# Optimization experiments

Hardware: AMD Instinct MI355X
Metric: run time of the kernel (lower is better)

The kernel has to match this reference:

```python
import jax, jax.numpy as jnp
import numpy as np


def _maxpool3(x):
    # 3x3 max pool, stride 1, SAME padding (NHWC), matches tf.keras MaxPooling2D
    return jax.lax.reduce_window(
        x, -jnp.inf, jax.lax.max,
        window_dimensions=(1, 3, 3, 1),
        window_strides=(1, 1, 1, 1),
        padding='SAME')


def setup_inputs() -> dict:
    key = jax.random.key(0)
    scores = jax.random.uniform(key, (16, 1024, 1024, 1), dtype=jnp.float32)
    return {"scores": scores}


def reference(scores):
    zeros = jnp.zeros_like(scores)
    max_mask = scores == _maxpool3(scores)
    for _ in range(2):
        supp_mask = _maxpool3(max_mask.astype(scores.dtype)) > 0
        supp_scores = jnp.where(supp_mask, zeros, scores)
        new_max_mask = supp_scores == _maxpool3(supp_scores)
        max_mask = max_mask | (new_max_mask & ~supp_mask)
    return jnp.where(max_mask, scores, zeros)
```

## Files before the change

### kernel.cpp

```cpp
#include <hip/hip_runtime.h>

#define IMG 1024
#define RH  16
#define NW  4
#define NEG_INF (-__builtin_inff())
#define PMASK 0x01010101u

__device__ __forceinline__ unsigned dpp_shr1_u(unsigned x) {
    return (unsigned)__builtin_amdgcn_update_dpp(0, (int)x, 0x138, 0xf, 0xf, true);
}
__device__ __forceinline__ unsigned dpp_shl1_u(unsigned x) {
    return (unsigned)__builtin_amdgcn_update_dpp(0, (int)x, 0x130, 0xf, 0xf, true);
}
__device__ __forceinline__ float dpp_shr1_f(float x) { return __uint_as_float(dpp_shr1_u(__float_as_uint(x))); }
__device__ __forceinline__ float dpp_shl1_f(float x) { return __uint_as_float(dpp_shl1_u(__float_as_uint(x))); }

__device__ __forceinline__ float max3f(float a, float b, float c) { return fmaxf(fmaxf(a, b), c); }

__device__ __forceinline__ float4 vmax3(float4 a, float4 b, float4 c) {
    return make_float4(max3f(a.x,b.x,c.x), max3f(a.y,b.y,c.y),
                       max3f(a.z,b.z,c.z), max3f(a.w,b.w,c.w));
}

__device__ __forceinline__ float4 hmax3(float4 f, float Lin, float Rin, bool l0, bool l63) {
    float sl = dpp_shr1_f(f.w);
    float sr = dpp_shl1_f(f.x);
    float L = l0 ? Lin : sl;
    float R = l63 ? Rin : sr;
    return make_float4(max3f(L,   f.x, f.y), max3f(f.x, f.y, f.z),
                       max3f(f.y, f.z, f.w), max3f(f.z, f.w, R));
}

__device__ __forceinline__ unsigned hor3(unsigned p, unsigned Lbit, unsigned Rbit, bool l0, bool l63) {
    unsigned sl = dpp_shr1_u(p);
    unsigned sr = dpp_shl1_u(p);
    unsigned L = l0 ? Lbit : ((sl >> 24) & 1u);
    unsigned R = l63 ? Rbit : (sr & 1u);
    return ((p | (p << 8) | (p >> 8)) & PMASK) | L | (R << 24);
}

__device__ __forceinline__ unsigned cmp_plane(float4 a, float4 m) {
    return (a.x == m.x ? 0x1u : 0u) | (a.y == m.y ? 0x100u : 0u) |
           (a.z == m.z ? 0x10000u : 0u) | (a.w == m.w ? 0x1000000u : 0u);
}

__device__ __forceinline__ float4 supsel(unsigned plane, float4 v) {
    return make_float4(((plane >>  0) & 1u) ? 0.f : v.x,
                       ((plane >>  8) & 1u) ? 0.f : v.y,
                       ((plane >> 16) & 1u) ? 0.f : v.z,
                       ((plane >> 24) & 1u) ? 0.f : v.w);
}

__device__ __forceinline__ float bsel(unsigned bits, int sh, float v) {
    return ((bits >> sh) & 1u) ? v : 0.f;
}

__device__ __forceinline__ unsigned vmask(int r, int lmax) {
    return ((unsigned)r < (unsigned)lmax) ? PMASK : 0u;
}

#define LDS_BARRIER() do {                                   \
    __builtin_amdgcn_sched_barrier(0);                       \
    asm volatile("s_waitcnt lgkmcnt(0)" ::: "memory");       \
    __builtin_amdgcn_s_barrier();                            \
    __builtin_amdgcn_sched_barrier(0);                       \
} while (0)

#define STEP(K, PAR) do {                                                               \
    const int s_ = sb + (K);                                                            \
    const float4 pLp = edgeR[(PAR)^1][w];                                               \
    const float4 pRp = edgeL[(PAR)^1][w + 2];                                           \
    const unsigned pLb = __float_as_uint(pLp.w);                                        \
    const unsigned pRb = __float_as_uint(pRp.w);                                        \
                                                          \
    HV[(K)+2] = hmax3(H[9+(K)], pLp.x, pRp.x, l0, l63);                                 \
                                                                    \
    float4 vm0 = vmax3(HV[(K)+2], HV[(K)+1], HV[(K)]);                                  \
    unsigned m0n = cmp_plane(H[8+(K)], vm0) & vmask(s_ - 2, lmax);                      \
    m0h = ((m0h << 1) & ~PMASK) | m0n;                                                  \
                                                                   \
    unsigned hm0n = hor3((m0h >> 1) & PMASK, pLb & 1u, pRb & 1u, l0, l63);              \
    hm0h = ((hm0h << 1) & ~PMASK) | hm0n;                                               \
                                                                 \
    unsigned s1n = (hm0h | (hm0h >> 1) | (hm0h >> 2)) & PMASK;                          \
    s1h = ((s1h << 1) & ~PMASK) | s1n;                                                  \
        \
    SS1[(K)+2] = supsel(s1n & vmask(s_ - 4, lmax), H[6+(K)]);                           \
                                                             \
    H1[(K)+2] = hmax3(SS1[(K)+1], pLp.y, pRp.y, l0, l63);                               \
                                                                 \
    float4 vm1 = vmax3(H1[(K)+2], H1[(K)+1], H1[(K)]);                                  \
    unsigned s1l2 = (s1h >> 2) & PMASK;                                                 \
    unsigned rvm6 = vmask(s_ - 6, lmax);                                                \
    unsigned nm1 = cmp_plane(SS1[(K)], vm1) & rvm6;                                     \
    unsigned mk1n = ((m0h >> 4) & PMASK) | (nm1 & ~s1l2);                               \
    mk1h = ((mk1h << 1) & ~PMASK) | mk1n;                                               \
                                                                  \
    unsigned hm1n = hor3((mk1h >> 1) & PMASK, (pLb >> 1) & 1u, (pRb >> 1) & 1u, l0, l63);\
    hm1h = ((hm1h << 1) & ~PMASK) | hm1n;                                               \
                                                                \
    unsigned s2n = (hm1h | (hm1h >> 1) | (hm1h >> 2)) & PMASK;                          \
    s2h = ((s2h << 1) & ~PMASK) | s2n;                                                  \
                           \
    SS2[(K)+2] = supsel(s2n & vmask(s_ - 8, lmax), H[2+(K)]);                           \
                                                            \
    H2[(K)+2] = hmax3(SS2[(K)+1], pLp.z, pRp.z, l0, l63);                               \
                                                      \
    float4 vm2 = vmax3(H2[(K)+2], H2[(K)+1], H2[(K)]);                                  \
    unsigned s2l2 = (s2h >> 2) & PMASK;                                                 \
    unsigned rvm10 = vmask(s_ - 10, lmax);                                              \
    unsigned nm2 = cmp_plane(SS2[(K)], vm2) & rvm10;                                    \
    unsigned mk2 = ((mk1h >> 4) & PMASK) | (nm2 & ~s2l2);                               \
    const int srow = s_ - 10;                                                           \
    if (srow >= y0 && srow < yend) {                                                    \
        float4 vv = H[(K)];                                                             \
        outp4[(size_t)srow * (IMG/4) + tid] = make_float4(                              \
            bsel(mk2, 0, vv.x), bsel(mk2, 8, vv.y),                                     \
            bsel(mk2, 16, vv.z), bsel(mk2, 24, vv.w));                                  \
    }                                                                                   \
    unsigned bitsR = ((m0n >> 24) & 1u) | (((mk1n >> 24) & 1u) << 1);                   \
    unsigned bitsL = (m0n & 1u) | ((mk1n & 1u) << 1);                                   \
    if (l63) edgeR[(PAR)][w + 1] = make_float4(H[10+(K)].w, SS1[(K)+2].w, SS2[(K)+2].w, __uint_as_float(bitsR)); \
    if (l0)  edgeL[(PAR)][w + 1] = make_float4(H[10+(K)].x, SS1[(K)+2].x, SS2[(K)+2].x, __uint_as_float(bitsL)); \
    LDS_BARRIER();                                                                      \
} while (0)

__global__ __launch_bounds__(256, 4)
void nms_sweep(const float* __restrict__ in, float* __restrict__ out)
{
    __shared__ float4 edgeR[2][NW + 2];
    __shared__ float4 edgeL[2][NW + 2];

    const int tid  = threadIdx.x;
    const int lane = tid & 63;
    const int w    = tid >> 6;
    const bool l0  = (lane == 0);
    const bool l63 = (lane == 63);
    const int y0   = (int)blockIdx.x * RH;
    const int yend = y0 + RH;
    const size_t base = (size_t)blockIdx.y * ((size_t)IMG * IMG);
    const int lmax = (yend + 5 < IMG) ? yend + 5 : IMG;

    const float4* inp4  = (const float4*)(in + base);
    float4*       outp4 = (float4*)(out + base);

    for (int i = tid; i < 2 * (NW + 2); i += 256) {
        int p = i & 1, sl = i >> 1;
        float4 s = make_float4(NEG_INF, NEG_INF, NEG_INF, __uint_as_float(0u));
        edgeR[p][sl] = s;
        edgeL[p][sl] = s;
    }

    const float4 ninf4 = make_float4(NEG_INF, NEG_INF, NEG_INF, NEG_INF);
    float4 H[14], HV[6], SS1[6], H1[6], SS2[6], H2[6];
#pragma unroll
    for (int i = 0; i < 14; ++i) H[i] = ninf4;
#pragma unroll
    for (int i = 0; i < 6; ++i) { HV[i] = ninf4; H1[i] = ninf4; H2[i] = ninf4; SS1[i] = ninf4; SS2[i] = ninf4; }
    unsigned m0h = 0, hm0h = 0, s1h = 0, mk1h = 0, hm1h = 0, s2h = 0;

    int sb = y0 - 5;
    __syncthreads();

    for (int it = 0; it < (RH + 15 + 3) / 4; ++it) {
#pragma unroll
        for (int k = 0; k < 4; ++k) {
            const int r = sb + k;
            H[10 + k] = ((unsigned)r < (unsigned)lmax) ? inp4[(size_t)r * (IMG/4) + tid] : ninf4;
        }

        STEP(0, 1);
        STEP(1, 0);
        STEP(2, 1);
        STEP(3, 0);

#pragma unroll
        for (int i = 0; i < 10; ++i) H[i] = H[i + 4];
        HV[0] = HV[4];   HV[1] = HV[5];
        SS1[0] = SS1[4]; SS1[1] = SS1[5];
        H1[0] = H1[4];   H1[1] = H1[5];
        SS2[0] = SS2[4]; SS2[1] = SS2[5];
        H2[0] = H2[4];   H2[1] = H2[5];
        sb += 4;
    }
}

extern "C" void kernel_launch(void* const* d_in, const int* in_sizes, int n_in,
                              void* d_out, int out_size, void* d_ws, size_t ws_size,
                              hipStream_t stream) {
    const float* in = (const float*)d_in[0];
    float* out = (float*)d_out;
    const int batch = in_sizes[0] / (IMG * IMG);
    dim3 grid(IMG / RH, batch, 1);
    nms_sweep<<<grid, dim3(256, 1, 1), 0, stream>>>(in, out);
}
```

Baseline: 54.98 us.

## Replace LDS halo exchange with overlapping per-wave column strips and prefetch

Each wave now independently processes a 256-column strip (stepping by 240 columns with an 8-column overlap on each side) instead of four waves sharing a full row through LDS edge exchange and per-row barriers. This removes all shared memory traffic and block-wide barriers, at the cost of redundant loads and computation on the overlapping halo columns (five strips cover the 1024-wide row). The band height is doubled to amortize vertical halo rows, and the next four input rows are software-prefetched into registers while the current ones are processed, with launch bounds relaxed to two blocks per SM to accommodate the extra registers.

```diff
diff --git a/kernel.cpp b/kernel.cpp
--- a/kernel.cpp
+++ b/kernel.cpp
@@ -1,8 +1,9 @@
 #include <hip/hip_runtime.h>
 
 #define IMG 1024
-#define RH  16
-#define NW  4
+#define RH  32
+#define NBANDS (IMG / RH)
+#define NSTRIP 5
 #define NEG_INF (-__builtin_inff())
 #define PMASK 0x01010101u
 
@@ -22,21 +23,19 @@
                        max3f(a.z,b.z,c.z), max3f(a.w,b.w,c.w));
 }
 
-__device__ __forceinline__ float4 hmax3(float4 f, float Lin, float Rin, bool l0, bool l63) {
+__device__ __forceinline__ float4 hmax3(float4 f, bool l0, bool l63) {
     float sl = dpp_shr1_f(f.w);
     float sr = dpp_shl1_f(f.x);
-    float L = l0 ? Lin : sl;
-    float R = l63 ? Rin : sr;
+    float L = l0  ? NEG_INF : sl;
+    float R = l63 ? NEG_INF : sr;
     return make_float4(max3f(L,   f.x, f.y), max3f(f.x, f.y, f.z),
                        max3f(f.y, f.z, f.w), max3f(f.z, f.w, R));
 }
 
-__device__ __forceinline__ unsigned hor3(unsigned p, unsigned Lbit, unsigned Rbit, bool l0, bool l63) {
+__device__ __forceinline__ unsigned hor3(unsigned p) {
     unsigned sl = dpp_shr1_u(p);
     unsigned sr = dpp_shl1_u(p);
-    unsigned L = l0 ? Lbit : ((sl >> 24) & 1u);
-    unsigned R = l63 ? Rbit : (sr & 1u);
-    return ((p | (p << 8) | (p >> 8)) & PMASK) | L | (R << 24);
+    return ((p | (p << 8) | (p >> 8)) & PMASK) | ((sl >> 24) & 1u) | ((sr & 1u) << 24);
 }
 
 __device__ __forceinline__ unsigned cmp_plane(float4 a, float4 m) {
@@ -59,100 +58,84 @@
     return ((unsigned)r < (unsigned)lmax) ? PMASK : 0u;
 }
 
-#define LDS_BARRIER() do {                                   \
-    __builtin_amdgcn_sched_barrier(0);                       \
-    asm volatile("s_waitcnt lgkmcnt(0)" ::: "memory");       \
-    __builtin_amdgcn_s_barrier();                            \
-    __builtin_amdgcn_sched_barrier(0);                       \
-} while (0)
-
-#define STEP(K, PAR) do {                                                               \
+#define STEP(K) do {                                                                    \
     const int s_ = sb + (K);                                                            \
-    const float4 pLp = edgeR[(PAR)^1][w];                                               \
-    const float4 pRp = edgeL[(PAR)^1][w + 2];                                           \
-    const unsigned pLb = __float_as_uint(pLp.w);                                        \
-    const unsigned pRb = __float_as_uint(pRp.w);                                        \
                                                           \
-    HV[(K)+2] = hmax3(H[9+(K)], pLp.x, pRp.x, l0, l63);                                 \
+    HV[(K)+2] = hmax3(H[9+(K)], l0, l63);                                               \
                                                                     \
     float4 vm0 = vmax3(HV[(K)+2], HV[(K)+1], HV[(K)]);                                  \
     unsigned m0n = cmp_plane(H[8+(K)], vm0) & vmask(s_ - 2, lmax);                      \
     m0h = ((m0h << 1) & ~PMASK) | m0n;                                                  \
                                                                    \
-    unsigned hm0n = hor3((m0h >> 1) & PMASK, pLb & 1u, pRb & 1u, l0, l63);              \
+    unsigned hm0n = hor3((m0h >> 1) & PMASK);                                           \
     hm0h = ((hm0h << 1) & ~PMASK) | hm0n;                                               \
                                                                  \
     unsigned s1n = (hm0h | (hm0h >> 1) | (hm0h >> 2)) & PMASK;                          \
     s1h = ((s1h << 1) & ~PMASK) | s1n;                                                  \
-        \
+                      \
     SS1[(K)+2] = supsel(s1n & vmask(s_ - 4, lmax), H[6+(K)]);                           \
                                                              \
-    H1[(K)+2] = hmax3(SS1[(K)+1], pLp.y, pRp.y, l0, l63);                               \
+    H1[(K)+2] = hmax3(SS1[(K)+1], l0, l63);                                             \
                                                                  \
     float4 vm1 = vmax3(H1[(K)+2], H1[(K)+1], H1[(K)]);                                  \
     unsigned s1l2 = (s1h >> 2) & PMASK;                                                 \
-    unsigned rvm6 = vmask(s_ - 6, lmax);                                                \
-    unsigned nm1 = cmp_plane(SS1[(K)], vm1) & rvm6;                                     \
+    unsigned nm1 = cmp_plane(SS1[(K)], vm1) & vmask(s_ - 6, lmax);                      \
     unsigned mk1n = ((m0h >> 4) & PMASK) | (nm1 & ~s1l2);                               \
     mk1h = ((mk1h << 1) & ~PMASK) | mk1n;                                               \
                                                                   \
-    unsigned hm1n = hor3((mk1h >> 1) & PMASK, (pLb >> 1) & 1u, (pRb >> 1) & 1u, l0, l63);\
+    unsigned hm1n = hor3((mk1h >> 1) & PMASK);                                          \
     hm1h = ((hm1h << 1) & ~PMASK) | hm1n;                                               \
                                                                 \
     unsigned s2n = (hm1h | (hm1h >> 1) | (hm1h >> 2)) & PMASK;                          \
     s2h = ((s2h << 1) & ~PMASK) | s2n;                                                  \
-                           \
+                                                 \
     SS2[(K)+2] = supsel(s2n & vmask(s_ - 8, lmax), H[2+(K)]);                           \
                                                             \
-    H2[(K)+2] = hmax3(SS2[(K)+1], pLp.z, pRp.z, l0, l63);                               \
+    H2[(K)+2] = hmax3(SS2[(K)+1], l0, l63);                                             \
                                                       \
     float4 vm2 = vmax3(H2[(K)+2], H2[(K)+1], H2[(K)]);                                  \
     unsigned s2l2 = (s2h >> 2) & PMASK;                                                 \
-    unsigned rvm10 = vmask(s_ - 10, lmax);                                              \
-    unsigned nm2 = cmp_plane(SS2[(K)], vm2) & rvm10;                                    \
+    unsigned nm2 = cmp_plane(SS2[(K)], vm2) & vmask(s_ - 10, lmax);                     \
     unsigned mk2 = ((mk1h >> 4) & PMASK) | (nm2 & ~s2l2);                               \
     const int srow = s_ - 10;                                                           \
-    if (srow >= y0 && srow < yend) {                                                    \
+    if (srow >= y0 && srow < yend && ok_lane) {                                         \
         float4 vv = H[(K)];                                                             \
-        outp4[(size_t)srow * (IMG/4) + tid] = make_float4(                              \
+        outp4[(size_t)srow * (IMG/4) + cb4 + lane] = make_float4(                       \
             bsel(mk2, 0, vv.x), bsel(mk2, 8, vv.y),                                     \
             bsel(mk2, 16, vv.z), bsel(mk2, 24, vv.w));                                  \
     }                                                                                   \
-    unsigned bitsR = ((m0n >> 24) & 1u) | (((mk1n >> 24) & 1u) << 1);                   \
-    unsigned bitsL = (m0n & 1u) | ((mk1n & 1u) << 1);                                   \
-    if (l63) edgeR[(PAR)][w + 1] = make_float4(H[10+(K)].w, SS1[(K)+2].w, SS2[(K)+2].w, __uint_as_float(bitsR)); \
-    if (l0)  edgeL[(PAR)][w + 1] = make_float4(H[10+(K)].x, SS1[(K)+2].x, SS2[(K)+2].x, __uint_as_float(bitsL)); \
-    LDS_BARRIER();                                                                      \
 } while (0)
 
-__global__ __launch_bounds__(256, 4)
+__global__ __launch_bounds__(256, 2)
 void nms_sweep(const float* __restrict__ in, float* __restrict__ out)
 {
-    __shared__ float4 edgeR[2][NW + 2];
-    __shared__ float4 edgeL[2][NW + 2];
-
     const int tid  = threadIdx.x;
     const int lane = tid & 63;
     const int w    = tid >> 6;
     const bool l0  = (lane == 0);
     const bool l63 = (lane == 63);
-    const int y0   = (int)blockIdx.x * RH;
-    const int yend = y0 + RH;
+
+    const int wid   = (int)blockIdx.x * 4 + w;
+    const int strip = wid / NBANDS;
+    const int band  = wid - strip * NBANDS;
+    const int y0    = band * RH;
+    const int yend  = y0 + RH;
+    const int cb    = strip * 240;
+    const int cb4   = cb >> 2;
     const size_t base = (size_t)blockIdx.y * ((size_t)IMG * IMG);
-    const int lmax = (yend + 5 < IMG) ? yend + 5 : IMG;
+    const int lmax  = (yend + 5 < IMG) ? yend + 5 : IMG;
 
     const float4* inp4  = (const float4*)(in + base);
     float4*       outp4 = (float4*)(out + base);
 
-    for (int i = tid; i < 2 * (NW + 2); i += 256) {
-        int p = i & 1, sl = i >> 1;
-        float4 s = make_float4(NEG_INF, NEG_INF, NEG_INF, __uint_as_float(0u));
-        edgeR[p][sl] = s;
-        edgeL[p][sl] = s;
-    }
+    const int lc = cb + 4 * lane;
+    const bool col_ok = lc < IMG;
+    const int lo_off = (strip == 0) ? 0 : 8;
+    const int hi_off = (IMG - cb < 248) ? (IMG - cb) : 248;
+    const bool ok_lane = (4 * lane >= lo_off) && (4 * lane + 4 <= hi_off);
 
     const float4 ninf4 = make_float4(NEG_INF, NEG_INF, NEG_INF, NEG_INF);
-    float4 H[14], HV[6], SS1[6], H1[6], SS2[6], H2[6];
+    float4 H[14], Hn[4], HV[6], SS1[6], H1[6], SS2[6], H2[6];
 #pragma unroll
     for (int i = 0; i < 14; ++i) H[i] = ninf4;
 #pragma unroll
@@ -160,22 +143,28 @@
     unsigned m0h = 0, hm0h = 0, s1h = 0, mk1h = 0, hm1h = 0, s2h = 0;
 
     int sb = y0 - 5;
-    __syncthreads();
+
+#pragma unroll
+    for (int k = 0; k < 4; ++k) {
+        const int r = sb + k;
+        H[10 + k] = (col_ok && (unsigned)r < (unsigned)lmax) ? inp4[(size_t)r * (IMG/4) + cb4 + lane] : ninf4;
+    }
 
     for (int it = 0; it < (RH + 15 + 3) / 4; ++it) {
 #pragma unroll
         for (int k = 0; k < 4; ++k) {
-            const int r = sb + k;
-            H[10 + k] = ((unsigned)r < (unsigned)lmax) ? inp4[(size_t)r * (IMG/4) + tid] : ninf4;
+            const int r = sb + 4 + k;
+            Hn[k] = (col_ok && (unsigned)r < (unsigned)lmax) ? inp4[(size_t)r * (IMG/4) + cb4 + lane] : ninf4;
         }
 
-        STEP(0, 1);
-        STEP(1, 0);
-        STEP(2, 1);
-        STEP(3, 0);
+        STEP(0);
+        STEP(1);
+        STEP(2);
+        STEP(3);
 
 #pragma unroll
         for (int i = 0; i < 10; ++i) H[i] = H[i + 4];
+        H[10] = Hn[0]; H[11] = Hn[1]; H[12] = Hn[2]; H[13] = Hn[3];
         HV[0] = HV[4];   HV[1] = HV[5];
         SS1[0] = SS1[4]; SS1[1] = SS1[5];
         H1[0] = H1[4];   H1[1] = H1[5];
@@ -191,6 +180,6 @@
     const float* in = (const float*)d_in[0];
     float* out = (float*)d_out;
     const int batch = in_sizes[0] / (IMG * IMG);
-    dim3 grid(IMG / RH, batch, 1);
+    dim3 grid((NSTRIP * NBANDS) / 4, batch, 1);
     nms_sweep<<<grid, dim3(256, 1, 1), 0, stream>>>(in, out);
 }
```

Result: faster. 53.09 us (-3.4%).
